# Optimization experiments

Hardware: AMD Instinct MI355X
Metric: run time of the kernel (lower is better)

Reference implementation:

```python
import jax, jax.numpy as jnp
import numpy as np

NEG_SLOPE = 0.01  # torch nn.LeakyReLU default


def setup_inputs() -> dict:
    key = jax.random.key(0)
    k1, k2, k3, k4, k5 = jax.random.split(key, 5)
    B, C, N, O = 32, 512, 1024, 512
    x = jax.random.normal(k1, (B, C, N), dtype=jnp.float32)
    wq = jax.random.normal(k2, (C,), dtype=jnp.float32) * (1.0 / np.sqrt(C))
    wk = jax.random.normal(k3, (C,), dtype=jnp.float32) * (1.0 / np.sqrt(C))
    wm = jax.random.normal(k4, (O, C), dtype=jnp.float32) * (1.0 / np.sqrt(C))
    bm = jax.random.normal(k5, (O,), dtype=jnp.float32) * 0.01
    return {"x": x, "wq": wq, "wk": wk, "wm": wm, "bm": bm}


def reference(x, wq, wk, wm, bm):
    # x: [B, C, N]
    q = jnp.einsum('c,bcn->bn', wq, x)            # [B, N] (Conv1d C->1, k=1, no bias)
    k = jnp.einsum('c,bcn->bn', wk, x)            # [B, N]
    scores = q[:, None, :] + k[:, :, None]        # [B, N, N] additive broadcast
    scores = jnp.where(scores > 0, scores, NEG_SLOPE * scores)  # LeakyReLU
    att = jax.nn.softmax(scores, axis=-1)         # softmax over last dim
    agg = jnp.einsum('bcn,bmn->bcm', x, att)      # weighted aggregation [B, C, N]
    out = jnp.einsum('oc,bcm->bom', wm, agg) + bm[None, :, None]  # Conv1d k=1
    return jax.nn.relu(out)
```

## Files before the change

### kernel.cpp

```cpp
#include <hip/hip_runtime.h>


constexpr int B = 32, C = 512, N = 1024, O = 512;
constexpr float L2E = 1.4426950408889634f;

typedef _Float16 half8 __attribute__((ext_vector_type(8)));
typedef _Float16 half4v __attribute__((ext_vector_type(4)));
typedef _Float16 half2v __attribute__((ext_vector_type(2)));
typedef float f32x4 __attribute__((ext_vector_type(4)));

#if __has_builtin(__builtin_amdgcn_exp2f)
#define EXP2(x) __builtin_amdgcn_exp2f(x)
#else
#define EXP2(x) exp2f(x)
#endif

__device__ __forceinline__ half8 cvt8(float4 a, float4 b) {
  half8 h;
  h[0] = (_Float16)a.x; h[1] = (_Float16)a.y; h[2] = (_Float16)a.z; h[3] = (_Float16)a.w;
  h[4] = (_Float16)b.x; h[5] = (_Float16)b.y; h[6] = (_Float16)b.z; h[7] = (_Float16)b.w;
  return h;
}

__global__ __launch_bounds__(256) void qk_kernel(const float* __restrict__ x,
    const float* __restrict__ wq, const float* __restrict__ wk,
    float* __restrict__ q, float* __restrict__ k) {
  int b = blockIdx.y;
  int l = threadIdx.x & 63;
  int cq = threadIdx.x >> 6;
  int n = blockIdx.x * 64 + l;
  const float* xp  = x + ((size_t)b * C + cq * 128) * N + n;
  const float* wqp = wq + cq * 128;
  const float* wkp = wk + cq * 128;
  float aq = 0.f, ak = 0.f;
#pragma unroll 8
  for (int c = 0; c < 128; ++c) {
    float v = xp[(size_t)c * N];
    aq += wqp[c] * v;
    ak += wkp[c] * v;
  }
  __shared__ float rq[4][64], rk[4][64];
  rq[cq][l] = aq;
  rk[cq][l] = ak;
  __syncthreads();
  if (threadIdx.x < 64) {
    float sq = (rq[0][l] + rq[1][l]) + (rq[2][l] + rq[3][l]);
    float sk = (rk[0][l] + rk[1][l]) + (rk[2][l] + rk[3][l]);
    q[b * N + blockIdx.x * 64 + l] = L2E * sq;
    k[b * N + blockIdx.x * 64 + l] = L2E * sk;
  }
}

__global__ __launch_bounds__(256) void qmax_kernel(const float* __restrict__ q,
                                                   float* __restrict__ qmax) {
  int b = blockIdx.x;
  int tid = threadIdx.x;
  float m = -1e30f;
  for (int n = tid; n < N; n += 256) m = fmaxf(m, q[b * N + n]);
#pragma unroll
  for (int off = 32; off > 0; off >>= 1) m = fmaxf(m, __shfl_down(m, off, 64));
  __shared__ float red[4];
  if ((tid & 63) == 0) red[tid >> 6] = m;
  __syncthreads();
  if (tid == 0) qmax[b] = fmaxf(fmaxf(red[0], red[1]), fmaxf(red[2], red[3]));
}

__global__ __launch_bounds__(256) void gemm_y_kernel(const float* __restrict__ x,
    const float* __restrict__ wm, _Float16* __restrict__ Yt) {
  __shared__ half2v Xs[16 * 130];
  __shared__ __align__(16) _Float16 Ws[128 * 40];
  int b  = blockIdx.y;
  int n0 = blockIdx.x * 128;
  int o0 = blockIdx.z * 128;
  int t = threadIdx.x;
  int w = t >> 6, l = t & 63;
  int nw = w >> 1, ow = w & 1;
  int lm = l & 15, q8 = (l >> 4) * 8, q4 = (l >> 4) * 4;

  int cp = t >> 4, ng = t & 15;
  int wrow = t >> 2, woff = (t & 3) * 8;

  f32x4 acc[4][4] = {};
  for (int c0 = 0; c0 < C; c0 += 32) {
    const float* xr = x + ((size_t)b * C + c0 + 2 * cp) * N + n0 + ng * 8;
    float4 a0 = *(const float4*)(xr);
    float4 a1 = *(const float4*)(xr + 4);
    float4 b0 = *(const float4*)(xr + N);
    float4 b1 = *(const float4*)(xr + N + 4);
    const float* wr = wm + (size_t)(o0 + wrow) * C + c0 + woff;
    float4 w0 = *(const float4*)(wr);
    float4 w1 = *(const float4*)(wr + 4);
    float4 w2 = *(const float4*)(wr + (size_t)64 * C);
    float4 w3 = *(const float4*)(wr + (size_t)64 * C + 4);
    __syncthreads();
    {
      half2v* xp = &Xs[cp * 130 + ng * 8];
      xp[0] = half2v{(_Float16)a0.x, (_Float16)b0.x};
      xp[1] = half2v{(_Float16)a0.y, (_Float16)b0.y};
      xp[2] = half2v{(_Float16)a0.z, (_Float16)b0.z};
      xp[3] = half2v{(_Float16)a0.w, (_Float16)b0.w};
      xp[4] = half2v{(_Float16)a1.x, (_Float16)b1.x};
      xp[5] = half2v{(_Float16)a1.y, (_Float16)b1.y};
      xp[6] = half2v{(_Float16)a1.z, (_Float16)b1.z};
      xp[7] = half2v{(_Float16)a1.w, (_Float16)b1.w};
      *(half8*)&Ws[wrow * 40 + woff]        = cvt8(w0, w1);
      *(half8*)&Ws[(wrow + 64) * 40 + woff] = cvt8(w2, w3);
    }
    __syncthreads();

    half8 af[4], bf[4];
#pragma unroll
    for (int i = 0; i < 4; ++i) {
      int nrow = nw * 64 + i * 16 + lm;
#pragma unroll
      for (int jp = 0; jp < 4; ++jp) {
        half2v p = Xs[(q4 + jp) * 130 + nrow];
        af[i][2 * jp]     = p[0];
        af[i][2 * jp + 1] = p[1];
      }
    }
#pragma unroll
    for (int j = 0; j < 4; ++j)
      bf[j] = *(const half8*)&Ws[(ow * 64 + j * 16 + lm) * 40 + q8];
#pragma unroll
    for (int i = 0; i < 4; ++i)
#pragma unroll
      for (int j = 0; j < 4; ++j)
        acc[i][j] = __builtin_amdgcn_mfma_f32_16x16x32_f16(af[i], bf[j], acc[i][j], 0, 0, 0);
  }

#pragma unroll
  for (int i = 0; i < 4; ++i) {
    int n_b = n0 + nw * 64 + i * 16 + (l >> 4) * 4;
#pragma unroll
    for (int j = 0; j < 4; ++j) {
      int o_c = o0 + ow * 64 + j * 16 + lm;
      half4v h;
      h[0] = (_Float16)acc[i][j][0];
      h[1] = (_Float16)acc[i][j][1];
      h[2] = (_Float16)acc[i][j][2];
      h[3] = (_Float16)acc[i][j][3];
      *(half4v*)&Yt[((size_t)b * O + o_c) * N + n_b] = h;
    }
  }
}

__global__ __launch_bounds__(256) void gemm_out_kernel(const _Float16* __restrict__ Yt,
    const float* __restrict__ q, const float* __restrict__ k,
    const float* __restrict__ qmax, const float* __restrict__ bm,
    float* __restrict__ out) {
  __shared__ __align__(16) float qs[N];
  __shared__ __align__(16) _Float16 Es[128 * 40];
  __shared__ __align__(16) _Float16 Ys[128 * 40];
  __shared__ float izs[128];
  int b  = blockIdx.y;
  int o0 = blockIdx.x * 128;
  int m0 = blockIdx.z * 128;
  int t = threadIdx.x;
  int w = t >> 6, l = t & 63;
  int mw = w >> 1, ow = w & 1;
  int lm = l & 15, q8 = (l >> 4) * 8;

  *(float4*)&qs[t * 4] = *(const float4*)&q[b * N + t * 4];

  int m_l = t >> 1, nh = t & 1;
  float km = k[b * N + m0 + m_l];
  float qmv = qmax[b];
  float s0 = qmv + km;
  float M  = fmaxf(s0, 0.01f * s0);
  float k2 = km - M;
  float k3 = fmaf(0.01f, km, -M);
  float Zp = 0.f;
  int yrow = t >> 2, yoff = (t & 3) * 8;
  __syncthreads();

  f32x4 acc[4][4] = {};
  for (int n0k = 0; n0k < N; n0k += 32) {
    half8 y0 = *(const half8*)&Yt[((size_t)b * O + o0 + yrow) * N + n0k + yoff];
    half8 y1 = *(const half8*)&Yt[((size_t)b * O + o0 + yrow + 64) * N + n0k + yoff];
    float4 qv0 = *(const float4*)&qs[n0k + nh * 16];
    float4 qv1 = *(const float4*)&qs[n0k + nh * 16 + 4];
    float4 qv2 = *(const float4*)&qs[n0k + nh * 16 + 8];
    float4 qv3 = *(const float4*)&qs[n0k + nh * 16 + 12];
    float ev[16];
    {
      const float* qq = (const float*)&qv0;
      float tmp[16] = {qv0.x, qv0.y, qv0.z, qv0.w, qv1.x, qv1.y, qv1.z, qv1.w,
                       qv2.x, qv2.y, qv2.z, qv2.w, qv3.x, qv3.y, qv3.z, qv3.w};
      (void)qq;
#pragma unroll
      for (int jj = 0; jj < 16; ++jj) {
        float arg = fmaxf(tmp[jj] + k2, fmaf(0.01f, tmp[jj], k3));
        ev[jj] = EXP2(arg);
        Zp += ev[jj];
      }
    }
    half8 h0, h1;
#pragma unroll
    for (int jj = 0; jj < 8; ++jj) { h0[jj] = (_Float16)ev[jj]; h1[jj] = (_Float16)ev[jj + 8]; }

    __syncthreads();
    *(half8*)&Es[m_l * 40 + nh * 16]     = h0;
    *(half8*)&Es[m_l * 40 + nh * 16 + 8] = h1;
    *(half8*)&Ys[yrow * 40 + yoff]        = y0;
    *(half8*)&Ys[(yrow + 64) * 40 + yoff] = y1;
    __syncthreads();

    half8 af[4], bf[4];
#pragma unroll
    for (int i = 0; i < 4; ++i)
      af[i] = *(const half8*)&Es[(mw * 64 + i * 16 + lm) * 40 + q8];
#pragma unroll
    for (int j = 0; j < 4; ++j)
      bf[j] = *(const half8*)&Ys[(ow * 64 + j * 16 + lm) * 40 + q8];
#pragma unroll
    for (int i = 0; i < 4; ++i)
#pragma unroll
      for (int j = 0; j < 4; ++j)
        acc[i][j] = __builtin_amdgcn_mfma_f32_16x16x32_f16(af[i], bf[j], acc[i][j], 0, 0, 0);
  }

  float Z = Zp + __shfl_xor(Zp, 1, 64);
  izs[m_l] = 1.0f / Z;
  __syncthreads();

#pragma unroll
  for (int i = 0; i < 4; ++i) {
    int m_b = m0 + mw * 64 + i * 16 + (l >> 4) * 4;
    float4 iz4 = *(const float4*)&izs[mw * 64 + i * 16 + (l >> 4) * 4];
#pragma unroll
    for (int j = 0; j < 4; ++j) {
      int o_c = o0 + ow * 64 + j * 16 + lm;
      float bias = bm[o_c];
      float4 r;
      r.x = fmaxf(fmaf(acc[i][j][0], iz4.x, bias), 0.f);
      r.y = fmaxf(fmaf(acc[i][j][1], iz4.y, bias), 0.f);
      r.z = fmaxf(fmaf(acc[i][j][2], iz4.z, bias), 0.f);
      r.w = fmaxf(fmaf(acc[i][j][3], iz4.w, bias), 0.f);
      *(float4*)&out[((size_t)b * O + o_c) * N + m_b] = r;
    }
  }
}

extern "C" void kernel_launch(void* const* d_in, const int* in_sizes, int n_in,
                              void* d_out, int out_size, void* d_ws, size_t ws_size,
                              hipStream_t stream) {
  const float* x  = (const float*)d_in[0];
  const float* wq = (const float*)d_in[1];
  const float* wk = (const float*)d_in[2];
  const float* wm = (const float*)d_in[3];
  const float* bm = (const float*)d_in[4];
  float* out = (float*)d_out;

  float* q    = (float*)d_ws;
  float* k    = q + B * N;
  float* qmax = k + B * N;
  _Float16* Yt = (_Float16*)(qmax + 64);

  qk_kernel<<<dim3(N / 64, B), 256, 0, stream>>>(x, wq, wk, q, k);
  qmax_kernel<<<dim3(B), 256, 0, stream>>>(q, qmax);
  gemm_y_kernel<<<dim3(N / 128, B, O / 128), 256, 0, stream>>>(x, wm, Yt);
  gemm_out_kernel<<<dim3(O / 128, B, N / 128), 256, 0, stream>>>(Yt, q, k, qmax, bm, out);
}
```

Measured before the change: 228.9 us.

## Fuse q/k projection into Y GEMM and compute softmax fragments in registers

The q/k projection kernel is folded into the first GEMM: blocks with blockIdx.z==0 accumulate the wq/wk dot products from the x tiles they already load, then reduce them through shared memory. This removes a separate full pass over x. In the output GEMM, each lane now computes its exp weights directly in MFMA A-fragment layout and loads Y fragments straight from global memory. That removes the shared-memory staging and the two barriers per k-step. In exchange, each exp is computed twice (once per ow half), the z==0 blocks do extra work, and Y is loaded from global without reuse across warps.

```diff
diff --git a/kernel.cpp b/kernel.cpp
--- a/kernel.cpp
+++ b/kernel.cpp
@@ -22,51 +22,10 @@
   return h;
 }
 
-__global__ __launch_bounds__(256) void qk_kernel(const float* __restrict__ x,
-    const float* __restrict__ wq, const float* __restrict__ wk,
-    float* __restrict__ q, float* __restrict__ k) {
-  int b = blockIdx.y;
-  int l = threadIdx.x & 63;
-  int cq = threadIdx.x >> 6;
-  int n = blockIdx.x * 64 + l;
-  const float* xp  = x + ((size_t)b * C + cq * 128) * N + n;
-  const float* wqp = wq + cq * 128;
-  const float* wkp = wk + cq * 128;
-  float aq = 0.f, ak = 0.f;
-#pragma unroll 8
-  for (int c = 0; c < 128; ++c) {
-    float v = xp[(size_t)c * N];
-    aq += wqp[c] * v;
-    ak += wkp[c] * v;
-  }
-  __shared__ float rq[4][64], rk[4][64];
-  rq[cq][l] = aq;
-  rk[cq][l] = ak;
-  __syncthreads();
-  if (threadIdx.x < 64) {
-    float sq = (rq[0][l] + rq[1][l]) + (rq[2][l] + rq[3][l]);
-    float sk = (rk[0][l] + rk[1][l]) + (rk[2][l] + rk[3][l]);
-    q[b * N + blockIdx.x * 64 + l] = L2E * sq;
-    k[b * N + blockIdx.x * 64 + l] = L2E * sk;
-  }
-}
-
-__global__ __launch_bounds__(256) void qmax_kernel(const float* __restrict__ q,
-                                                   float* __restrict__ qmax) {
-  int b = blockIdx.x;
-  int tid = threadIdx.x;
-  float m = -1e30f;
-  for (int n = tid; n < N; n += 256) m = fmaxf(m, q[b * N + n]);
-#pragma unroll
-  for (int off = 32; off > 0; off >>= 1) m = fmaxf(m, __shfl_down(m, off, 64));
-  __shared__ float red[4];
-  if ((tid & 63) == 0) red[tid >> 6] = m;
-  __syncthreads();
-  if (tid == 0) qmax[b] = fmaxf(fmaxf(red[0], red[1]), fmaxf(red[2], red[3]));
-}
-
 __global__ __launch_bounds__(256) void gemm_y_kernel(const float* __restrict__ x,
-    const float* __restrict__ wm, _Float16* __restrict__ Yt) {
+    const float* __restrict__ wm, const float* __restrict__ wq,
+    const float* __restrict__ wk, float* __restrict__ q, float* __restrict__ k,
+    _Float16* __restrict__ Yt) {
   __shared__ half2v Xs[16 * 130];
   __shared__ __align__(16) _Float16 Ws[128 * 40];
   int b  = blockIdx.y;
@@ -79,6 +38,8 @@
 
   int cp = t >> 4, ng = t & 15;
   int wrow = t >> 2, woff = (t & 3) * 8;
+  bool doqk = (blockIdx.z == 0);
+  float aq[8] = {}, ak[8] = {};
 
   f32x4 acc[4][4] = {};
   for (int c0 = 0; c0 < C; c0 += 32) {
@@ -92,6 +53,28 @@
     float4 w1 = *(const float4*)(wr + 4);
     float4 w2 = *(const float4*)(wr + (size_t)64 * C);
     float4 w3 = *(const float4*)(wr + (size_t)64 * C + 4);
+
+    if (doqk) {
+      float2 wq2 = *(const float2*)&wq[c0 + 2 * cp];
+      float2 wk2 = *(const float2*)&wk[c0 + 2 * cp];
+      aq[0] = fmaf(wq2.x, a0.x, fmaf(wq2.y, b0.x, aq[0]));
+      aq[1] = fmaf(wq2.x, a0.y, fmaf(wq2.y, b0.y, aq[1]));
+      aq[2] = fmaf(wq2.x, a0.z, fmaf(wq2.y, b0.z, aq[2]));
+      aq[3] = fmaf(wq2.x, a0.w, fmaf(wq2.y, b0.w, aq[3]));
+      aq[4] = fmaf(wq2.x, a1.x, fmaf(wq2.y, b1.x, aq[4]));
+      aq[5] = fmaf(wq2.x, a1.y, fmaf(wq2.y, b1.y, aq[5]));
+      aq[6] = fmaf(wq2.x, a1.z, fmaf(wq2.y, b1.z, aq[6]));
+      aq[7] = fmaf(wq2.x, a1.w, fmaf(wq2.y, b1.w, aq[7]));
+      ak[0] = fmaf(wk2.x, a0.x, fmaf(wk2.y, b0.x, ak[0]));
+      ak[1] = fmaf(wk2.x, a0.y, fmaf(wk2.y, b0.y, ak[1]));
+      ak[2] = fmaf(wk2.x, a0.z, fmaf(wk2.y, b0.z, ak[2]));
+      ak[3] = fmaf(wk2.x, a0.w, fmaf(wk2.y, b0.w, ak[3]));
+      ak[4] = fmaf(wk2.x, a1.x, fmaf(wk2.y, b1.x, ak[4]));
+      ak[5] = fmaf(wk2.x, a1.y, fmaf(wk2.y, b1.y, ak[5]));
+      ak[6] = fmaf(wk2.x, a1.z, fmaf(wk2.y, b1.z, ak[6]));
+      ak[7] = fmaf(wk2.x, a1.w, fmaf(wk2.y, b1.w, ak[7]));
+    }
+
     __syncthreads();
     {
       half2v* xp = &Xs[cp * 130 + ng * 8];
@@ -143,6 +126,44 @@
       *(half4v*)&Yt[((size_t)b * O + o_c) * N + n_b] = h;
     }
   }
+
+  if (doqk) {
+    float* red = (float*)Ws;
+    __syncthreads();
+#pragma unroll
+    for (int j = 0; j < 8; ++j) red[cp * 132 + ng * 8 + j] = aq[j];
+    __syncthreads();
+    if (t < 128) {
+      float s = 0.f;
+#pragma unroll
+      for (int p = 0; p < 16; ++p) s += red[p * 132 + t];
+      q[b * N + n0 + t] = L2E * s;
+    }
+    __syncthreads();
+#pragma unroll
+    for (int j = 0; j < 8; ++j) red[cp * 132 + ng * 8 + j] = ak[j];
+    __syncthreads();
+    if (t < 128) {
+      float s = 0.f;
+#pragma unroll
+      for (int p = 0; p < 16; ++p) s += red[p * 132 + t];
+      k[b * N + n0 + t] = L2E * s;
+    }
+  }
+}
+
+__global__ __launch_bounds__(256) void qmax_kernel(const float* __restrict__ q,
+                                                   float* __restrict__ qmax) {
+  int b = blockIdx.x;
+  int tid = threadIdx.x;
+  float m = -1e30f;
+  for (int n = tid; n < N; n += 256) m = fmaxf(m, q[b * N + n]);
+#pragma unroll
+  for (int off = 32; off > 0; off >>= 1) m = fmaxf(m, __shfl_down(m, off, 64));
+  __shared__ float red[4];
+  if ((tid & 63) == 0) red[tid >> 6] = m;
+  __syncthreads();
+  if (tid == 0) qmax[b] = fmaxf(fmaxf(red[0], red[1]), fmaxf(red[2], red[3]));
 }
 
 __global__ __launch_bounds__(256) void gemm_out_kernel(const _Float16* __restrict__ Yt,
@@ -150,8 +171,6 @@
     const float* __restrict__ qmax, const float* __restrict__ bm,
     float* __restrict__ out) {
   __shared__ __align__(16) float qs[N];
-  __shared__ __align__(16) _Float16 Es[128 * 40];
-  __shared__ __align__(16) _Float16 Ys[128 * 40];
   __shared__ float izs[128];
   int b  = blockIdx.y;
   int o0 = blockIdx.x * 128;
@@ -159,75 +178,65 @@
   int t = threadIdx.x;
   int w = t >> 6, l = t & 63;
   int mw = w >> 1, ow = w & 1;
-  int lm = l & 15, q8 = (l >> 4) * 8;
+  int lm = l & 15, g = l >> 4, q8 = g * 8;
 
   *(float4*)&qs[t * 4] = *(const float4*)&q[b * N + t * 4];
 
-  int m_l = t >> 1, nh = t & 1;
-  float km = k[b * N + m0 + m_l];
   float qmv = qmax[b];
-  float s0 = qmv + km;
-  float M  = fmaxf(s0, 0.01f * s0);
-  float k2 = km - M;
-  float k3 = fmaf(0.01f, km, -M);
-  float Zp = 0.f;
-  int yrow = t >> 2, yoff = (t & 3) * 8;
+  float k2[4], k3[4];
+#pragma unroll
+  for (int i = 0; i < 4; ++i) {
+    float km = k[b * N + m0 + mw * 64 + i * 16 + lm];
+    float s0 = qmv + km;
+    float M  = fmaxf(s0, 0.01f * s0);
+    k2[i] = km - M;
+    k3[i] = fmaf(0.01f, km, -M);
+  }
+  float Zp[4] = {0.f, 0.f, 0.f, 0.f};
+  const _Float16* ybase = Yt + ((size_t)b * O + o0 + ow * 64 + lm) * N + q8;
   __syncthreads();
 
   f32x4 acc[4][4] = {};
+#pragma unroll 2
   for (int n0k = 0; n0k < N; n0k += 32) {
-    half8 y0 = *(const half8*)&Yt[((size_t)b * O + o0 + yrow) * N + n0k + yoff];
-    half8 y1 = *(const half8*)&Yt[((size_t)b * O + o0 + yrow + 64) * N + n0k + yoff];
-    float4 qv0 = *(const float4*)&qs[n0k + nh * 16];
-    float4 qv1 = *(const float4*)&qs[n0k + nh * 16 + 4];
-    float4 qv2 = *(const float4*)&qs[n0k + nh * 16 + 8];
-    float4 qv3 = *(const float4*)&qs[n0k + nh * 16 + 12];
-    float ev[16];
-    {
-      const float* qq = (const float*)&qv0;
-      float tmp[16] = {qv0.x, qv0.y, qv0.z, qv0.w, qv1.x, qv1.y, qv1.z, qv1.w,
-                       qv2.x, qv2.y, qv2.z, qv2.w, qv3.x, qv3.y, qv3.z, qv3.w};
-      (void)qq;
-#pragma unroll
-      for (int jj = 0; jj < 16; ++jj) {
-        float arg = fmaxf(tmp[jj] + k2, fmaf(0.01f, tmp[jj], k3));
-        ev[jj] = EXP2(arg);
-        Zp += ev[jj];
+    half8 bf[4];
+#pragma unroll
+    for (int j = 0; j < 4; ++j)
+      bf[j] = *(const half8*)(ybase + (size_t)(j * 16) * N + n0k);
+    float4 qa = *(const float4*)&qs[n0k + q8];
+    float4 qb = *(const float4*)&qs[n0k + q8 + 4];
+    float qv[8] = {qa.x, qa.y, qa.z, qa.w, qb.x, qb.y, qb.z, qb.w};
+#pragma unroll
+    for (int i = 0; i < 4; ++i) {
+      half8 af;
+      float zz = 0.f;
+#pragma unroll
+      for (int jj = 0; jj < 8; ++jj) {
+        float arg = fmaxf(qv[jj] + k2[i], fmaf(0.01f, qv[jj], k3[i]));
+        float e = EXP2(arg);
+        zz += e;
+        af[jj] = (_Float16)e;
       }
-    }
-    half8 h0, h1;
-#pragma unroll
-    for (int jj = 0; jj < 8; ++jj) { h0[jj] = (_Float16)ev[jj]; h1[jj] = (_Float16)ev[jj + 8]; }
-
-    __syncthreads();
-    *(half8*)&Es[m_l * 40 + nh * 16]     = h0;
-    *(half8*)&Es[m_l * 40 + nh * 16 + 8] = h1;
-    *(half8*)&Ys[yrow * 40 + yoff]        = y0;
-    *(half8*)&Ys[(yrow + 64) * 40 + yoff] = y1;
-    __syncthreads();
-
-    half8 af[4], bf[4];
-#pragma unroll
-    for (int i = 0; i < 4; ++i)
-      af[i] = *(const half8*)&Es[(mw * 64 + i * 16 + lm) * 40 + q8];
-#pragma unroll
-    for (int j = 0; j < 4; ++j)
-      bf[j] = *(const half8*)&Ys[(ow * 64 + j * 16 + lm) * 40 + q8];
-#pragma unroll
-    for (int i = 0; i < 4; ++i)
+      Zp[i] += zz;
 #pragma unroll
       for (int j = 0; j < 4; ++j)
-        acc[i][j] = __builtin_amdgcn_mfma_f32_16x16x32_f16(af[i], bf[j], acc[i][j], 0, 0, 0);
-  }
-
-  float Z = Zp + __shfl_xor(Zp, 1, 64);
-  izs[m_l] = 1.0f / Z;
+        acc[i][j] = __builtin_amdgcn_mfma_f32_16x16x32_f16(af, bf[j], acc[i][j], 0, 0, 0);
+    }
+  }
+
+#pragma unroll
+  for (int i = 0; i < 4; ++i) {
+    float z = Zp[i];
+    z += __shfl_xor(z, 16, 64);
+    z += __shfl_xor(z, 32, 64);
+    if (ow == 0 && g == 0) izs[mw * 64 + i * 16 + lm] = 1.0f / z;
+  }
   __syncthreads();
 
 #pragma unroll
   for (int i = 0; i < 4; ++i) {
-    int m_b = m0 + mw * 64 + i * 16 + (l >> 4) * 4;
-    float4 iz4 = *(const float4*)&izs[mw * 64 + i * 16 + (l >> 4) * 4];
+    int m_b = m0 + mw * 64 + i * 16 + g * 4;
+    float4 iz4 = *(const float4*)&izs[mw * 64 + i * 16 + g * 4];
 #pragma unroll
     for (int j = 0; j < 4; ++j) {
       int o_c = o0 + ow * 64 + j * 16 + lm;
@@ -257,8 +266,7 @@
   float* qmax = k + B * N;
   _Float16* Yt = (_Float16*)(qmax + 64);
 
-  qk_kernel<<<dim3(N / 64, B), 256, 0, stream>>>(x, wq, wk, q, k);
+  gemm_y_kernel<<<dim3(N / 128, B, O / 128), 256, 0, stream>>>(x, wm, wq, wk, q, k, Yt);
   qmax_kernel<<<dim3(B), 256, 0, stream>>>(q, qmax);
-  gemm_y_kernel<<<dim3(N / 128, B, O / 128), 256, 0, stream>>>(x, wm, Yt);
   gemm_out_kernel<<<dim3(O / 128, B, N / 128), 256, 0, stream>>>(Yt, q, k, qmax, bm, out);
 }
```

Result: slower. 234.9 us (+2.6%).
